# Performance work log

Measured on AMD Instinct MI355X. Metric: run time of the kernel, lower is better.

Reference implementation:

```python
import jax, jax.numpy as jnp
import numpy as np


def setup_inputs() -> dict:
    key = jax.random.key(0)
    k1, k2, k3 = jax.random.split(key, 3)
    T, H, F, E = 8192, 1024, 4096, 8
    x = jax.random.normal(k1, (T, H), dtype=jnp.float32)
    # expert weights, scaled like typical init (std ~ 1/sqrt(H))
    w1 = jax.random.normal(k2, (E, F, H), dtype=jnp.float32) * (1.0 / np.sqrt(H))
    w2 = jax.random.normal(k3, (E, F, H), dtype=jnp.float32) * (1.0 / np.sqrt(F))
    return {"x": x, "w1": w1, "w2": w2, "num_experts": E}


def reference(x, w1, w2, num_experts):
    # x: [T, H] tokens already permuted/grouped by expert (dMoE convention),
    # equal capacity per expert. w1, w2: [E, F, H].
    T, H = x.shape
    E = num_experts
    cap = T // E
    xe = x.reshape(E, cap, H)  # [E, cap, H]
    # sdd(x, w1.t(), topo): per-expert x_e @ w1_e^T -> [E, cap, F]
    h = jnp.einsum('ech,efh->ecf', xe, w1)
    # megablocks uses tanh-approximate gelu
    h = jax.nn.gelu(h, approximate=True)
    # dsd(gelu(h), w2): per-expert h_e @ w2_e -> [E, cap, H]
    out = jnp.einsum('ecf,efh->ech', h, w2)
    return out.reshape(T, H)
```

## Files before the change

### kernel.cpp

```cpp
#include <hip/hip_runtime.h>
#include <cstdint>
#include <cstddef>

typedef unsigned short u16;
typedef __attribute__((ext_vector_type(8))) short bf16x8;
typedef __attribute__((ext_vector_type(4))) float f32x4;
typedef __attribute__((ext_vector_type(8))) unsigned short u16x8;

#define T_TOK 8192
#define H_DIM 1024
#define F_DIM 4096
#define E_NUM 8
#define CAP (T_TOK / E_NUM)

template <int I> struct IC { static constexpr int v = I; };

__device__ __forceinline__ u16 f2bf(float f) {
  union { float f; uint32_t u; } v; v.f = f;
  uint32_t r = v.u + 0x7FFFu + ((v.u >> 16) & 1u);
  return (u16)(r >> 16);
}

__device__ __forceinline__ float gelu_tanh(float x) {
  float z2 = 1.5957691216057308f * (x + 0.044715f * x * x * x);
  float e = __expf(z2);
  return x * (1.0f - 1.0f / (e + 1.0f));
}

__device__ __forceinline__ void async_copy16(const void* gsrc, void* ldst) {
  __builtin_amdgcn_global_load_lds(
      (const __attribute__((address_space(1))) uint32_t*)gsrc,
      (__attribute__((address_space(3))) uint32_t*)ldst, 16, 0, 0);
}

__device__ __forceinline__ void wgbar() {
  asm volatile("" ::: "memory");
  __builtin_amdgcn_s_barrier();
  asm volatile("" ::: "memory");
}

template <int N> __device__ __forceinline__ void vm_wait() {
  if constexpr (N == 0) asm volatile("s_waitcnt vmcnt(0)" ::: "memory");
  else if constexpr (N == 3) asm volatile("s_waitcnt vmcnt(3)" ::: "memory");
  else if constexpr (N == 4) asm volatile("s_waitcnt vmcnt(4)" ::: "memory");
  else if constexpr (N == 6) asm volatile("s_waitcnt vmcnt(6)" ::: "memory");
  else if constexpr (N == 8) asm volatile("s_waitcnt vmcnt(8)" ::: "memory");
}

__device__ __forceinline__ void lgkm0() {
  asm volatile("s_waitcnt lgkmcnt(0)" ::: "memory");
}

__global__ __launch_bounds__(256) void k_convert(const float* __restrict__ src,
                                                 u16* __restrict__ dst, long n) {
  long i = ((long)blockIdx.x * 256 + threadIdx.x) * 8;
  long stride = (long)gridDim.x * 256 * 8;
  for (; i < n; i += stride) {
    const float4 a = *(const float4*)(src + i);
    const float4 b = *(const float4*)(src + i + 4);
    u16x8 o;
    o[0] = f2bf(a.x); o[1] = f2bf(a.y); o[2] = f2bf(a.z); o[3] = f2bf(a.w);
    o[4] = f2bf(b.x); o[5] = f2bf(b.y); o[6] = f2bf(b.z); o[7] = f2bf(b.w);
    *(u16x8*)(dst + i) = o;
  }
}

__global__ __launch_bounds__(256) void k_transpose_w2(const float* __restrict__ w2,
                                                      u16* __restrict__ w2t) {
  __shared__ float tile[32][33];
  const int ntH = H_DIM / 32;
  const int ntF = F_DIM / 32;
  int bid = blockIdx.x;
  int e = bid / (ntF * ntH);
  int r = bid % (ntF * ntH);
  int f0 = (r / ntH) * 32;
  int h0 = (r % ntH) * 32;
  const float* src = w2 + (size_t)e * F_DIM * H_DIM;
  u16* dst = w2t + (size_t)e * H_DIM * F_DIM;
  int col = threadIdx.x & 31;
  int row8 = threadIdx.x >> 5;
#pragma unroll
  for (int i = 0; i < 4; i++) {
    int row = row8 + i * 8;
    tile[row][col] = src[(size_t)(f0 + row) * H_DIM + h0 + col];
  }
  __syncthreads();
#pragma unroll
  for (int i = 0; i < 4; i++) {
    int row = row8 + i * 8;
    dst[(size_t)(h0 + row) * F_DIM + f0 + col] = f2bf(tile[col][row]);
  }
}

template <int BN, int WM, int WN, int NTN, int NT, bool GELU, int NPH>
__global__ __launch_bounds__(512, 2) void k_gemm(const u16* __restrict__ Ag,
                                                 const u16* __restrict__ Bg,
                                                 void* __restrict__ Cg) {
  constexpr int K = NT * 64;
  constexpr int WROWS = 256 / WM;
  constexpr int WCOLS = BN / WN;
  constexpr int FM = WROWS / 16;
  constexpr int FN = WCOLS / 16;
  constexpr int AH = (NPH == 4) ? FM / 2 : FM;
  constexpr int PA = 256 * 32;
  constexpr int PB = BN * 32;
  constexpr int ABOFF = 4 * PA;
  constexpr int JA = 2;
  constexpr int JB = BN / 128;
  constexpr int VMS = 2 * (JA + JB);
  constexpr int VMH = JA + JB;
  constexpr int NTOT = NTN * BN;
  constexpr int NTM = 32;

  __shared__ __align__(16) u16 lds[ABOFF + 4 * PB];

  const int tid = threadIdx.x;
  const int lane = tid & 63;
  const int wave = tid >> 6;
  const int wm = wave / WN;
  const int wn = wave % WN;

  constexpr int NWG = NTM * NTN;
  const int wg = ((int)blockIdx.x & 7) * (NWG / 8) + ((int)blockIdx.x >> 3);
  constexpr int NSN = NTN / 4;
  const int sup = wg >> 4, win = wg & 15;
  const int mt = (sup / NSN) * 4 + (win >> 2);
  const int nt_ = (sup % NSN) * 4 + (win & 3);

  const int e = mt >> 2;
  const u16* Ae = Ag + (size_t)mt * 256 * K;
  const u16* Be = Bg + (size_t)e * NTOT * K + (size_t)nt_ * BN * K;

  const int srow = lane >> 2;
  const int kswz = (((lane & 3) ^ ((lane >> 3) & 3)) << 3);
  const u16* srcA[JA];
  int dstA[JA];
  const u16* srcB[JB];
  int dstB[JB];
#pragma unroll
  for (int j = 0; j < JA; ++j) {
    const int cr = (JA * wave + j) * 16 + srow;
    srcA[j] = Ae + (size_t)cr * K + kswz;
    dstA[j] = (JA * wave + j) * 512;
  }
#pragma unroll
  for (int j = 0; j < JB; ++j) {
    const int cr = (JB * wave + j) * 16 + srow;
    srcB[j] = Be + (size_t)cr * K + kswz;
    dstB[j] = (JB * wave + j) * 512;
  }

  auto stageA = [&](int t, int kh) {
    const int pc = (t & 1) * 2 + kh;
    const int koff = t * 64 + kh * 32;
#pragma unroll
    for (int j = 0; j < JA; ++j)
      async_copy16(srcA[j] + koff, &lds[pc * PA + dstA[j]]);
  };
  auto stageB = [&](int t, int kh) {
    const int pc = (t & 1) * 2 + kh;
    const int koff = t * 64 + kh * 32;
#pragma unroll
    for (int j = 0; j < JB; ++j)
      async_copy16(srcB[j] + koff, &lds[ABOFF + pc * PB + dstB[j]]);
  };

  const int frow = lane & 15;
  const int fslot = (((lane >> 4) ^ ((lane >> 1) & 3)) << 3);
  const int aoff = (wm * WROWS + frow) * 32 + fslot;
  const int boff = (wn * WCOLS + frow) * 32 + fslot;

  f32x4 acc[FM][FN] = {};
  bf16x8 af[AH], bf[FN];

  auto rdB = [&](int pc) {
    const u16* pb = &lds[ABOFF + pc * PB + boff];
#pragma unroll
    for (int j = 0; j < FN; ++j) bf[j] = *(const bf16x8*)(pb + j * 512);
  };
  auto rdA = [&](int pc, auto MH) {
    const u16* pa = &lds[pc * PA + aoff];
#pragma unroll
    for (int i = 0; i < AH; ++i)
      af[i] = *(const bf16x8*)(pa + (MH.v * AH + i) * 512);
  };
  auto mfmaC = [&](auto MH) {
    __builtin_amdgcn_s_setprio(1);
#pragma unroll
    for (int i = 0; i < AH; ++i)
#pragma unroll
      for (int j = 0; j < FN; ++j)
        acc[MH.v * AH + i][j] = __builtin_amdgcn_mfma_f32_16x16x32_bf16(
            af[i], bf[j], acc[MH.v * AH + i][j], 0, 0, 0);
    __builtin_amdgcn_s_setprio(0);
  };

  stageA(0, 0); stageB(0, 0);
  stageA(0, 1); stageB(0, 1);
  stageA(1, 0); stageB(1, 0);
  vm_wait<VMS>();
  wgbar();

  for (int t = 0; t < NT; ++t) {
    const int p0 = (t & 1) * 2, p1 = p0 + 1;
    if constexpr (NPH == 4) {
      rdB(p0); rdA(p0, IC<0>{});
      if (t < NT - 1) stageA(t + 1, 1);
      wgbar(); lgkm0();
      mfmaC(IC<0>{});
      wgbar();
      rdA(p0, IC<1>{});
      if (t < NT - 1) stageB(t + 1, 1);
      wgbar(); lgkm0();
      mfmaC(IC<1>{});
      if (t < NT - 1) vm_wait<VMS>(); else vm_wait<0>();
      wgbar();
      rdB(p1); rdA(p1, IC<0>{});
      if (t < NT - 2) stageA(t + 2, 0);
      wgbar(); lgkm0();
      mfmaC(IC<0>{});
      wgbar();
      rdA(p1, IC<1>{});
      if (t < NT - 2) stageB(t + 2, 0);
      wgbar(); lgkm0();
      mfmaC(IC<1>{});
      if (t < NT - 2) vm_wait<VMS>();
      else if (t == NT - 2) vm_wait<VMH>();
      wgbar();
    } else {
      rdB(p0); rdA(p0, IC<0>{});
      if (t < NT - 1) { stageA(t + 1, 1); stageB(t + 1, 1); }
      wgbar(); lgkm0();
      mfmaC(IC<0>{});
      if (t < NT - 1) vm_wait<VMS>(); else vm_wait<0>();
      wgbar();
      rdB(p1); rdA(p1, IC<0>{});
      if (t < NT - 2) { stageA(t + 2, 0); stageB(t + 2, 0); }
      wgbar(); lgkm0();
      mfmaC(IC<0>{});
      if (t < NT - 2) vm_wait<VMS>();
      else if (t == NT - 2) vm_wait<VMH>();
      wgbar();
    }
  }

  const int lr = (lane >> 4) * 4;
  const int lc = lane & 15;
  const size_t Crow0 = (size_t)mt * 256 + wm * WROWS;
  const int Ccol0 = nt_ * BN + wn * WCOLS;
#pragma unroll
  for (int fm = 0; fm < FM; ++fm)
#pragma unroll
    for (int fn = 0; fn < FN; ++fn) {
      const int col = Ccol0 + fn * 16 + lc;
#pragma unroll
      for (int r = 0; r < 4; ++r) {
        const size_t row = Crow0 + fm * 16 + lr + r;
        if constexpr (GELU) {
          ((u16*)Cg)[row * NTOT + col] = f2bf(gelu_tanh(acc[fm][fn][r]));
        } else {
          ((float*)Cg)[row * NTOT + col] = acc[fm][fn][r];
        }
      }
    }
}

extern "C" void kernel_launch(void* const* d_in, const int* in_sizes, int n_in,
                              void* d_out, int out_size, void* d_ws, size_t ws_size,
                              hipStream_t stream) {
  const float* x = (const float*)d_in[0];
  const float* w1 = (const float*)d_in[1];
  const float* w2 = (const float*)d_in[2];

  u16* ws_x = (u16*)d_ws;
  u16* ws_w1 = ws_x + (size_t)T_TOK * H_DIM;
  u16* ws_w2t = ws_w1 + (size_t)E_NUM * F_DIM * H_DIM;
  u16* ws_h = ws_w2t + (size_t)E_NUM * H_DIM * F_DIM;
  const size_t need =
      ((size_t)T_TOK * H_DIM + 2 * (size_t)E_NUM * F_DIM * H_DIM + (size_t)T_TOK * F_DIM) * 2;
  if (ws_size < need) return;

  k_convert<<<1024, 256, 0, stream>>>(x, ws_x, (long)T_TOK * H_DIM);
  k_convert<<<2048, 256, 0, stream>>>(w1, ws_w1, (long)E_NUM * F_DIM * H_DIM);
  k_transpose_w2<<<E_NUM * (F_DIM / 32) * (H_DIM / 32), 256, 0, stream>>>(w2, ws_w2t);

  k_gemm<256, 2, 4, 16, 16, true, 4><<<512, 512, 0, stream>>>(ws_x, ws_w1, ws_h);
  k_gemm<128, 4, 2, 8, 64, false, 2><<<256, 512, 0, stream>>>(ws_h, ws_w2t, d_out);
}
```

Measured before the change: 262.0 us.

## Double-buffer LDS fragment registers to overlap ds_reads with MFMA

Fragment registers for A and B become double-buffered, so the LDS reads for the next phase are issued before the current phase's MFMAs. Those MFMAs then wait only for their own operands through partial lgkmcnt waits instead of a full drain. One workgroup barrier per phase is removed, and the vmcnt thresholds are recomputed for the new staging order, with a conservative full drain over the last iterations. This roughly doubles fragment register use and depends on exact waitcnt accounting, so there is a risk of lower occupancy or subtle races.

Result: no change. 261.5 us (-0.2%).

```diff
diff --git a/kernel.cpp b/kernel.cpp
--- a/kernel.cpp
+++ b/kernel.cpp
@@ -40,15 +40,18 @@
 }
 
 template <int N> __device__ __forceinline__ void vm_wait() {
+  static_assert(N == 0 || N == 3 || N == 6 || N == 8, "vm_wait: unsupported N");
   if constexpr (N == 0) asm volatile("s_waitcnt vmcnt(0)" ::: "memory");
   else if constexpr (N == 3) asm volatile("s_waitcnt vmcnt(3)" ::: "memory");
-  else if constexpr (N == 4) asm volatile("s_waitcnt vmcnt(4)" ::: "memory");
   else if constexpr (N == 6) asm volatile("s_waitcnt vmcnt(6)" ::: "memory");
   else if constexpr (N == 8) asm volatile("s_waitcnt vmcnt(8)" ::: "memory");
 }
 
-__device__ __forceinline__ void lgkm0() {
-  asm volatile("s_waitcnt lgkmcnt(0)" ::: "memory");
+template <int N> __device__ __forceinline__ void lgkm_wait() {
+  static_assert(N == 0 || N == 4 || N == 8, "lgkm_wait: unsupported N");
+  if constexpr (N == 0) asm volatile("s_waitcnt lgkmcnt(0)" ::: "memory");
+  else if constexpr (N == 4) asm volatile("s_waitcnt lgkmcnt(4)" ::: "memory");
+  else if constexpr (N == 8) asm volatile("s_waitcnt lgkmcnt(8)" ::: "memory");
 }
 
 __global__ __launch_bounds__(256) void k_convert(const float* __restrict__ src,
@@ -107,8 +110,8 @@
   constexpr int ABOFF = 4 * PA;
   constexpr int JA = 2;
   constexpr int JB = BN / 128;
-  constexpr int VMS = 2 * (JA + JB);
-  constexpr int VMH = JA + JB;
+  constexpr int VMS = (NPH == 4) ? (2 * JA + JB) : (JA + JB);
+  constexpr int VMP = (NPH == 4) ? 8 : 3;
   constexpr int NTOT = NTN * BN;
   constexpr int NTM = 32;
 
@@ -171,75 +174,82 @@
   const int boff = (wn * WCOLS + frow) * 32 + fslot;
 
   f32x4 acc[FM][FN] = {};
-  bf16x8 af[AH], bf[FN];
-
-  auto rdB = [&](int pc) {
+  bf16x8 af2[2][AH], bf2[2][FN];
+
+  auto rdB = [&](auto BUF, int pc) {
     const u16* pb = &lds[ABOFF + pc * PB + boff];
 #pragma unroll
-    for (int j = 0; j < FN; ++j) bf[j] = *(const bf16x8*)(pb + j * 512);
-  };
-  auto rdA = [&](int pc, auto MH) {
+    for (int j = 0; j < FN; ++j) bf2[BUF.v][j] = *(const bf16x8*)(pb + j * 512);
+  };
+  auto rdA = [&](auto BUF, auto MH, int pc) {
     const u16* pa = &lds[pc * PA + aoff];
 #pragma unroll
     for (int i = 0; i < AH; ++i)
-      af[i] = *(const bf16x8*)(pa + (MH.v * AH + i) * 512);
-  };
-  auto mfmaC = [&](auto MH) {
+      af2[BUF.v][i] = *(const bf16x8*)(pa + (MH.v * AH + i) * 512);
+  };
+  auto mfmaC = [&](auto AB, auto BB, auto MH) {
     __builtin_amdgcn_s_setprio(1);
 #pragma unroll
     for (int i = 0; i < AH; ++i)
 #pragma unroll
       for (int j = 0; j < FN; ++j)
         acc[MH.v * AH + i][j] = __builtin_amdgcn_mfma_f32_16x16x32_bf16(
-            af[i], bf[j], acc[MH.v * AH + i][j], 0, 0, 0);
+            af2[AB.v][i], bf2[BB.v][j], acc[MH.v * AH + i][j], 0, 0, 0);
     __builtin_amdgcn_s_setprio(0);
   };
 
   stageA(0, 0); stageB(0, 0);
   stageA(0, 1); stageB(0, 1);
   stageA(1, 0); stageB(1, 0);
-  vm_wait<VMS>();
+  vm_wait<VMP>();
   wgbar();
+  rdB(IC<0>{}, 0); rdA(IC<0>{}, IC<0>{}, 0);
 
   for (int t = 0; t < NT; ++t) {
     const int p0 = (t & 1) * 2, p1 = p0 + 1;
+    const int p0n = ((t + 1) & 1) * 2;
+    const bool tailVM = (t >= NT - 3);
     if constexpr (NPH == 4) {
-      rdB(p0); rdA(p0, IC<0>{});
+      rdA(IC<1>{}, IC<1>{}, p0);
       if (t < NT - 1) stageA(t + 1, 1);
-      wgbar(); lgkm0();
-      mfmaC(IC<0>{});
-      wgbar();
-      rdA(p0, IC<1>{});
+      lgkm_wait<AH>();
+      __builtin_amdgcn_sched_barrier(0);
+      mfmaC(IC<0>{}, IC<0>{}, IC<0>{});
+      if (tailVM) vm_wait<0>(); else vm_wait<VMS>();
+      wgbar();
+      rdB(IC<1>{}, p1); rdA(IC<0>{}, IC<0>{}, p1);
       if (t < NT - 1) stageB(t + 1, 1);
-      wgbar(); lgkm0();
-      mfmaC(IC<1>{});
-      if (t < NT - 1) vm_wait<VMS>(); else vm_wait<0>();
-      wgbar();
-      rdB(p1); rdA(p1, IC<0>{});
+      lgkm_wait<AH + FN>();
+      __builtin_amdgcn_sched_barrier(0);
+      mfmaC(IC<1>{}, IC<0>{}, IC<1>{});
+      wgbar();
+      rdA(IC<1>{}, IC<1>{}, p1);
       if (t < NT - 2) stageA(t + 2, 0);
-      wgbar(); lgkm0();
-      mfmaC(IC<0>{});
-      wgbar();
-      rdA(p1, IC<1>{});
+      lgkm_wait<AH>();
+      __builtin_amdgcn_sched_barrier(0);
+      mfmaC(IC<0>{}, IC<1>{}, IC<0>{});
+      if (tailVM) vm_wait<0>(); else vm_wait<VMS>();
+      wgbar();
+      if (t < NT - 1) { rdB(IC<0>{}, p0n); rdA(IC<0>{}, IC<0>{}, p0n); }
       if (t < NT - 2) stageB(t + 2, 0);
-      wgbar(); lgkm0();
-      mfmaC(IC<1>{});
-      if (t < NT - 2) vm_wait<VMS>();
-      else if (t == NT - 2) vm_wait<VMH>();
+      if (t < NT - 1) lgkm_wait<AH + FN>(); else lgkm_wait<0>();
+      __builtin_amdgcn_sched_barrier(0);
+      mfmaC(IC<1>{}, IC<1>{}, IC<1>{});
       wgbar();
     } else {
-      rdB(p0); rdA(p0, IC<0>{});
+      rdB(IC<1>{}, p1); rdA(IC<1>{}, IC<0>{}, p1);
       if (t < NT - 1) { stageA(t + 1, 1); stageB(t + 1, 1); }
-      wgbar(); lgkm0();
-      mfmaC(IC<0>{});
-      if (t < NT - 1) vm_wait<VMS>(); else vm_wait<0>();
-      wgbar();
-      rdB(p1); rdA(p1, IC<0>{});
+      lgkm_wait<AH + FN>();
+      __builtin_amdgcn_sched_barrier(0);
+      mfmaC(IC<0>{}, IC<0>{}, IC<0>{});
+      if (tailVM) vm_wait<0>(); else vm_wait<VMS>();
+      wgbar();
+      if (t < NT - 1) { rdB(IC<0>{}, p0n); rdA(IC<0>{}, IC<0>{}, p0n); }
       if (t < NT - 2) { stageA(t + 2, 0); stageB(t + 2, 0); }
-      wgbar(); lgkm0();
-      mfmaC(IC<0>{});
-      if (t < NT - 2) vm_wait<VMS>();
-      else if (t == NT - 2) vm_wait<VMH>();
+      if (t < NT - 1) lgkm_wait<AH + FN>(); else lgkm_wait<0>();
+      __builtin_amdgcn_sched_barrier(0);
+      mfmaC(IC<1>{}, IC<1>{}, IC<0>{});
+      if (tailVM) vm_wait<0>(); else vm_wait<VMS>();
       wgbar();
     }
   }
```
